# Optimization experiments

Hardware: AMD Instinct MI355X
Metric: run time of the kernel (lower is better)

## Reference

```python
import jax, jax.numpy as jnp
import numpy as np
from math import factorial

N_NODES = 20000
N_EDGES = 80000
NUM_GRAPHS = 64
NUM_NEIGHBORS = 3.8
POOL_NODES = 4.0  # num_nodes=4 constant in source forward

# ---------------- real Wigner 3j (e3nn-style, Frobenius norm 1) ----------------

def _w3j_complex(j1, j2, j3, m1, m2, m3):
    if m1 + m2 + m3 != 0:
        return 0.0
    t1 = j2 - m1 - j3; t2 = j1 + m2 - j3; t3 = j1 + j2 - j3
    t4 = j1 - m1; t5 = j2 + m2
    tmin = max(0, t1, t2); tmax = min(t3, t4, t5)
    if tmin > tmax:
        return 0.0
    s = 0.0
    for t in range(tmin, tmax + 1):
        s += (-1.0) ** t / (factorial(t) * factorial(t - t1) * factorial(t - t2)
                            * factorial(t3 - t) * factorial(t4 - t) * factorial(t5 - t))
    tri = (factorial(j1 + j2 - j3) * factorial(j1 - j2 + j3) * factorial(-j1 + j2 + j3)
           / factorial(j1 + j2 + j3 + 1))
    norm = np.sqrt(tri * factorial(j1 + m1) * factorial(j1 - m1) * factorial(j2 + m2)
                   * factorial(j2 - m2) * factorial(j3 + m3) * factorial(j3 - m3))
    return (-1.0) ** (j1 - j2 - m3) * norm * s


def _real_basis(l):
    U = np.zeros((2 * l + 1, 2 * l + 1), dtype=np.complex128)
    U[l, l] = 1.0
    for m in range(1, l + 1):
        U[l + m, l + m] = (-1) ** m / np.sqrt(2.0)
        U[l + m, l - m] = 1.0 / np.sqrt(2.0)
        U[l - m, l - m] = 1j / np.sqrt(2.0)
        U[l - m, l + m] = -1j * (-1) ** m / np.sqrt(2.0)
    return U

_W3J_CACHE = {}

def w3j(l1, l2, l3):
    key = (l1, l2, l3)
    if key not in _W3J_CACHE:
        C = np.zeros((2 * l1 + 1, 2 * l2 + 1, 2 * l3 + 1), dtype=np.complex128)
        for m1 in range(-l1, l1 + 1):
            for m2 in range(-l2, l2 + 1):
                m3 = -(m1 + m2)
                if -l3 <= m3 <= l3:
                    C[m1 + l1, m2 + l2, m3 + l3] = _w3j_complex(l1, l2, l3, m1, m2, m3)
        C = np.einsum('ia,jb,kc,abc->ijk', _real_basis(l1), _real_basis(l2), _real_basis(l3), C)
        C = np.real((-1j) ** (l1 + l2 + l3) * C)
        _W3J_CACHE[key] = jnp.asarray(C, dtype=jnp.float32)
    return _W3J_CACHE[key]

# ---------------- irreps bookkeeping ----------------
SH        = [(1, 0, 1), (1, 1, -1), (1, 2, 1), (1, 3, -1)]            # 1x0e+1x1o+1x2e+1x3o (dim 16)
GATE1_IN  = [(16,0,1),(16,0,-1),(8,0,1),(8,0,-1),(8,0,1),(8,0,-1),(16,1,-1),(16,1,1)]  # dim 160
GATE1_OUT = [(16,0,1),(16,0,1),(16,1,-1),(16,1,1)]                     # dim 128
GATE2_IN  = [(16,0,1),(16,0,-1),(6,0,1),(6,0,-1),(6,0,1),(6,0,-1),(12,1,-1),(12,1,1)]  # dim 128
GATE2_OUT = [(16,0,1),(16,0,1),(12,1,-1),(12,1,1)]                     # dim 104
OUT_FINAL = [(1, 0, 1)]


def slices(irreps):
    out = []; o = 0
    for m, l, p in irreps:
        d = m * (2 * l + 1); out.append((o, o + d)); o += d
    return out


def tp_paths(ir1, ir2, iro):
    paths = []
    for i1, (m1, l1, p1) in enumerate(ir1):
        for i2, (m2, l2, p2) in enumerate(ir2):
            for io, (mo, lo, po) in enumerate(iro):
                if po == p1 * p2 and abs(l1 - l2) <= lo <= l1 + l2:
                    paths.append((i1, i2, io))
    fan = [0] * len(iro)
    for i1, i2, io in paths:
        fan[io] += ir1[i1][0] * ir2[i2][0]
    numel = sum(ir1[i1][0] * ir2[i2][0] * iro[io][0] for i1, i2, io in paths)
    return paths, fan, numel


def tensor_product(x1, x2, weights, ir1, ir2, iro):
    # FullyConnectedTensorProduct, component norm, element path normalization
    paths, fan, numel = tp_paths(ir1, ir2, iro)
    s1, s2 = slices(ir1), slices(ir2)
    E = x1.shape[0]
    out_parts = [jnp.zeros((E, m * (2 * l + 1)), x1.dtype) for m, l, p in iro]
    wofs = 0
    for i1, i2, io in paths:
        m1, l1, _ = ir1[i1]; m2, l2, _ = ir2[i2]; mo, lo, _ = iro[io]
        n = m1 * m2 * mo
        w = weights[:, wofs:wofs + n].reshape(E, m1, m2, mo); wofs += n
        a = x1[:, s1[i1][0]:s1[i1][1]].reshape(E, m1, 2 * l1 + 1)
        b = x2[:, s2[i2][0]:s2[i2][1]].reshape(E, m2, 2 * l2 + 1)
        C = w3j(l1, l2, lo)
        pw = np.sqrt((2 * lo + 1) / fan[io])
        seg = jnp.einsum('eui,evj,ijk,euvw->ewk', a, b, C, w) * pw
        out_parts[io] = out_parts[io] + seg.reshape(E, mo * (2 * lo + 1))
    return jnp.concatenate(out_parts, axis=1)

# ---------------- activations / gate ----------------
_xs = np.linspace(-8.0, 8.0, 100001)
_pdf = np.exp(-0.5 * _xs ** 2) / np.sqrt(2 * np.pi)
TANH_NORM = float(1.0 / np.sqrt(np.sum(np.tanh(_xs) ** 2 * _pdf) * (_xs[1] - _xs[0])))
SQRT2 = float(np.sqrt(2.0))
ACT = {'relu': lambda t: jnp.maximum(t, 0.0) * SQRT2,
       'abs':  lambda t: jnp.abs(t),
       'tanh': lambda t: jnp.tanh(t) * TANH_NORM}


def gate_fn(x, scalars, gates, gated):
    o = 0; outs = []
    for m, a in scalars:
        outs.append(ACT[a](x[:, o:o + m])); o += m
    gv = []
    for m, a in gates:
        gv.append(ACT[a](x[:, o:o + m])); o += m
    g = jnp.concatenate(gv, axis=-1)
    gi = 0
    for m, l in gated:
        d = 2 * l + 1
        feat = x[:, o:o + m * d].reshape(-1, m, d)
        outs.append((feat * g[:, gi:gi + m, None]).reshape(-1, m * d))
        o += m * d; gi += m
    return jnp.concatenate(outs, axis=-1)

# ---------------- edge features ----------------

def sh_component(v):
    # real spherical harmonics l=0..3, 'component' normalization, unit input
    x, y, z = v[:, 0], v[:, 1], v[:, 2]
    s3, s5, s15 = np.sqrt(3.0), np.sqrt(5.0), np.sqrt(15.0)
    s7, s42, s70, s105 = np.sqrt(7.0), np.sqrt(42.0), np.sqrt(70.0), np.sqrt(105.0)
    Y0 = jnp.ones_like(x)[:, None]
    Y1 = jnp.stack([s3 * y, s3 * z, s3 * x], -1)
    Y2 = jnp.stack([s15 * x * y, s15 * y * z, 0.5 * s5 * (3 * z * z - 1.0),
                    s15 * x * z, 0.5 * s15 * (x * x - y * y)], -1)
    Y3 = jnp.stack([0.25 * s70 * y * (3 * x * x - y * y), s105 * x * y * z,
                    0.25 * s42 * y * (5 * z * z - 1.0), 0.5 * s7 * z * (5 * z * z - 3.0),
                    0.25 * s42 * x * (5 * z * z - 1.0), 0.5 * s105 * z * (x * x - y * y),
                    0.25 * s70 * x * (x * x - 3 * y * y)], -1)
    return jnp.concatenate([Y0, Y1, Y2, Y3], -1)  # [E,16]


def soft_one_hot(r):
    # soft_one_hot_linspace(start=0.5,end=2.5,number=3,basis='smooth_finite',cutoff=True)
    values = np.linspace(0.5, 2.5, 5)[1:-1]
    step = values[1] - values[0]
    diff = (r[:, None] - values) / step
    def f(u):
        return jnp.where(u > 0, jnp.exp(-1.0 / jnp.where(u > 0, u, 1.0)), 0.0)
    y = 1.14136 * np.exp(2.0) * f(diff + 1.0) * f(1.0 - diff)
    return y * np.sqrt(3.0)


def fc(x, w1, w2):
    # e3nn FullyConnectedNet([3,256,numel], relu)
    h = jnp.maximum(x @ (w1 / np.sqrt(w1.shape[0])), 0.0) * SQRT2
    return h @ (w2 / np.sqrt(w2.shape[0]))


def convolution(node_feats, edge_src, edge_dst, edge_attr, edge_scalars, w1, w2, ir_in, ir_out, n_nodes):
    weight = fc(edge_scalars, w1, w2)                                   # [E, numel]
    ef = tensor_product(node_feats[edge_src], edge_attr, weight, ir_in, SH, ir_out)
    return jax.ops.segment_sum(ef, edge_dst, num_segments=n_nodes) / np.sqrt(NUM_NEIGHBORS)


def _forward(pos, w1_1, w2_1, w1_2, w2_2, w1_3, w2_3, edge_src, edge_dst, batch):
    N = pos.shape[0]
    vec = pos[edge_src] - pos[edge_dst]
    r = jnp.sqrt(jnp.sum(vec * vec, axis=1) + 1e-12)
    unit = vec / r[:, None]
    edge_attr = sh_component(unit)
    edge_scalars = soft_one_hot(r)
    x = jax.ops.segment_sum(edge_attr, edge_dst, num_segments=N) / np.sqrt(NUM_NEIGHBORS)
    x = convolution(x, edge_src, edge_dst, edge_attr, edge_scalars, w1_1, w2_1, SH, GATE1_IN, N)
    x = gate_fn(x, [(16, 'relu'), (16, 'abs')], [(8, 'relu'), (8, 'tanh'), (8, 'relu'), (8, 'tanh')], [(16, 1), (16, 1)])
    x = convolution(x, edge_src, edge_dst, edge_attr, edge_scalars, w1_2, w2_2, GATE1_OUT, GATE2_IN, N)
    x = gate_fn(x, [(16, 'relu'), (16, 'abs')], [(6, 'relu'), (6, 'tanh'), (6, 'relu'), (6, 'tanh')], [(12, 1), (12, 1)])
    x = convolution(x, edge_src, edge_dst, edge_attr, edge_scalars, w1_3, w2_3, GATE2_OUT, OUT_FINAL, N)
    x = jax.ops.segment_sum(x, batch, num_segments=NUM_GRAPHS) / np.sqrt(POOL_NODES)
    return jax.nn.sigmoid(x)


def setup_inputs():
    key = jax.random.key(0)
    ks = jax.random.split(key, 10)
    pos = jax.random.normal(ks[0], (N_NODES, 3), jnp.float32) * 1.5
    edge_src = jax.random.randint(ks[1], (N_EDGES,), 0, N_NODES)
    edge_dst = jax.random.randint(ks[2], (N_EDGES,), 0, N_NODES)
    batch = jnp.sort(jax.random.randint(ks[3], (N_NODES,), 0, NUM_GRAPHS))
    _, _, n1 = tp_paths(SH, SH, GATE1_IN)
    _, _, n2 = tp_paths(GATE1_OUT, SH, GATE2_IN)
    _, _, n3 = tp_paths(GATE2_OUT, SH, OUT_FINAL)
    w1_1 = jax.random.normal(ks[4], (3, 256), jnp.float32)
    w2_1 = jax.random.normal(ks[5], (256, n1), jnp.float32)
    w1_2 = jax.random.normal(ks[6], (3, 256), jnp.float32)
    w2_2 = jax.random.normal(ks[7], (256, n2), jnp.float32)
    w1_3 = jax.random.normal(ks[8], (3, 256), jnp.float32)
    w2_3 = jax.random.normal(ks[9], (256, n3), jnp.float32)
    return {'pos': pos, 'w1_1': w1_1, 'w2_1': w2_1, 'w1_2': w1_2, 'w2_2': w2_2,
            'w1_3': w1_3, 'w2_3': w2_3, 'edge_src': edge_src, 'edge_dst': edge_dst, 'batch': batch}


def reference(pos, w1_1, w2_1, w1_2, w2_2, w1_3, w2_3, edge_src, edge_dst, batch):
    return _forward(pos, w1_1, w2_1, w1_2, w2_2, w1_3, w2_3, edge_src, edge_dst, batch)
```

## Files before the change

### kernel.cpp

```cpp
#include <hip/hip_runtime.h>
#include <math.h>

#define NNODE 20000
#define NEDGE 80000
#define NGRAPH 64

#define OFF_TANH  656
#define OFF_CNT   660
#define OFF_GSUM  664
#define OFF_HIST  7680
#define OFF_OFFS  9728
#define OFF_CUR   11784
#define OFF_EATTR 14336
#define OFF_RBUF  1294336
#define OFF_EINFO 1374336
#define OFF_X0    1694336
#define OFF_Y1    2014336
#define OFF_Y2    5214336
#define OFF_X1    7774336
#define OFF_X2    10334336
#define OFF_TAB   12414336

#define T000 0
#define T110 1
#define T220 10
#define T330 35
#define T011 84
#define T101 93
#define T111 102
#define T121 129
#define T211 174
#define T231 219
#define T321 324
#define T221 429
#define T331 504

#define INV_SQRT_NEIGH 0.5129891760425771f
#define SQRT2F 1.4142135623730951f

struct TabD { int l1,l2,l3,off; };
constexpr TabD HTABS[13] = {
  {0,0,0,T000},{1,1,0,T110},{2,2,0,T220},{3,3,0,T330},
  {0,1,1,T011},{1,0,1,T101},{1,1,1,T111},{1,2,1,T121},
  {2,1,1,T211},{2,3,1,T231},{3,2,1,T321},{2,2,1,T221},{3,3,1,T331}
};

struct CoreD { short a_off, b_off; short l1,l2,l3; short tab; short coff; short m1; };
struct PathD { short core; short wofs, wend, ooff; short mo, lo; float pw; };

constexpr CoreD HCORES1[13] = {
  {0,0, 0,0,0, T000, 0, 1},
  {0,1, 0,1,1, T011, 1, 1},
  {1,0, 1,0,1, T101, 4, 1},
  {1,1, 1,1,0, T110, 7, 1},
  {1,1, 1,1,1, T111, 8, 1},
  {1,4, 1,2,1, T121, 11, 1},
  {4,1, 2,1,1, T211, 14, 1},
  {4,4, 2,2,0, T220, 17, 1},
  {4,4, 2,2,1, T221, 18, 1},
  {4,9, 2,3,1, T231, 21, 1},
  {9,4, 3,2,1, T321, 24, 1},
  {9,9, 3,3,0, T330, 27, 1},
  {9,9, 3,3,1, T331, 28, 1}
};
#define PWR 0.7071067811865476f
constexpr PathD HPATHS1[21] = {
  {0,  0, 16,  0,16,0,0.5f},
  {0, 16, 24, 32, 8,0,0.5f},
  {0, 24, 32, 48, 8,0,0.5f},
  {1, 32, 48, 64,16,1,PWR},
  {2, 48, 64, 64,16,1,PWR},
  {3, 64, 80,  0,16,0,0.5f},
  {3, 80, 88, 32, 8,0,0.5f},
  {3, 88, 96, 48, 8,0,0.5f},
  {4, 96,112,112,16,1,1.0f},
  {5,112,128, 64,16,1,PWR},
  {6,128,144, 64,16,1,PWR},
  {7,144,160,  0,16,0,0.5f},
  {7,160,168, 32, 8,0,0.5f},
  {7,168,176, 48, 8,0,0.5f},
  {8,176,192,112,16,1,1.0f},
  {9,192,208, 64,16,1,PWR},
  {10,208,224,64,16,1,PWR},
  {11,224,240, 0,16,0,0.5f},
  {11,240,248,32, 8,0,0.5f},
  {11,248,256,48, 8,0,0.5f},
  {12,256,272,112,16,1,1.0f}
};

constexpr CoreD HCORES2[12] = {
  {0,0,  0,0,0, T000, 0,   16},
  {0,1,  0,1,1, T011, 16,  16},
  {16,0, 0,0,0, T000, 64,  16},
  {16,1, 0,1,1, T011, 80,  16},
  {32,0, 1,0,1, T101, 128, 16},
  {32,1, 1,1,0, T110, 176, 16},
  {32,1, 1,1,1, T111, 192, 16},
  {32,4, 1,2,1, T121, 240, 16},
  {80,0, 1,0,1, T101, 288, 16},
  {80,1, 1,1,0, T110, 336, 16},
  {80,1, 1,1,1, T111, 352, 16},
  {80,4, 1,2,1, T121, 400, 16}
};
#define PA 0.14433756729740643f
#define PB 0.25f
#define PC 0.19364916731037085f
constexpr PathD HPATHS2[20] = {
  {0,   0, 256,  0,16,0,PA},
  {0, 256, 352, 32, 6,0,PA},
  {0, 352, 448, 44, 6,0,PA},
  {1, 448, 640, 56,12,1,PC},
  {2, 640, 896,  0,16,0,PA},
  {2, 896, 992, 32, 6,0,PA},
  {2, 992,1088, 44, 6,0,PA},
  {3,1088,1280, 56,12,1,PC},
  {4,1280,1472, 56,12,1,PC},
  {5,1472,1728,  0,16,0,PA},
  {5,1728,1824, 32, 6,0,PA},
  {5,1824,1920, 44, 6,0,PA},
  {6,1920,2112, 92,12,1,PB},
  {7,2112,2304, 56,12,1,PC},
  {8,2304,2496, 92,12,1,PB},
  {9,2496,2752, 16,16,0,PB},
  {9,2752,2848, 38, 6,0,PB},
  {9,2848,2944, 50, 6,0,PB},
  {10,2944,3136,56,12,1,PC},
  {11,3136,3328,92,12,1,PB}
};

constexpr CoreD HCORES3[3] = {
  {0,0,  0,0,0, T000, 0,  16},
  {16,0, 0,0,0, T000, 16, 16},
  {32,1, 1,1,0, T110, 32, 12}
};
#define PD 0.15075567228888181f
constexpr PathD HPATHS3[3] = {
  {0, 0,16, 0,1,0,PD},
  {1,16,32, 0,1,0,PD},
  {2,32,44, 0,1,0,PD}
};

constexpr double FACT[9] = {1.0,1.0,2.0,6.0,24.0,120.0,720.0,5040.0,40320.0};

constexpr double csqrt_(double x){
  if(x<=0.0) return 0.0;
  double g = (x<1.0)? 1.0 : x;
  for(int i=0;i<40;i++) g = 0.5*(g + x/g);
  return g;
}

constexpr double cw3j_(int j1,int j2,int j3,int m1,int m2,int m3){
  if(m1+m2+m3!=0) return 0.0;
  int t1=j2-m1-j3, t2=j1+m2-j3, t3=j1+j2-j3, t4=j1-m1, t5=j2+m2;
  int tmin=t1>0?t1:0; if(t2>tmin) tmin=t2;
  int tmax=t3<t4?t3:t4; if(t5<tmax) tmax=t5;
  if(tmin>tmax) return 0.0;
  double s=0.0;
  for(int t=tmin;t<=tmax;++t){
    double d=FACT[t]*FACT[t-t1]*FACT[t-t2]*FACT[t3-t]*FACT[t4-t]*FACT[t5-t];
    s += ((t&1)? -1.0:1.0)/d;
  }
  double tri=FACT[j1+j2-j3]*FACT[j1-j2+j3]*FACT[-j1+j2+j3]/FACT[j1+j2+j3+1];
  double nrm=csqrt_(tri*FACT[j1+m1]*FACT[j1-m1]*FACT[j2+m2]*FACT[j2-m2]*FACT[j3+m3]*FACT[j3-m3]);
  return (((j1-j2-m3)&1)? -1.0:1.0)*nrm*s;
}

constexpr int curow_(int l,int i,int* a,double* re,double* im){
  const double is2=0.7071067811865475;
  int m=i-l;
  if(m==0){ a[0]=l; re[0]=1.0; im[0]=0.0; return 1; }
  if(m>0){
    a[0]=l+m; re[0]=((m&1)? -is2:is2); im[0]=0.0;
    a[1]=l-m; re[1]=is2; im[1]=0.0; return 2;
  }
  int mm=-m;
  a[0]=l-mm; re[0]=0.0; im[0]=is2;
  a[1]=l+mm; re[1]=0.0; im[1]=((mm&1)? is2:-is2);
  return 2;
}

constexpr float cw3j_elem_(int l1,int l2,int l3,int i,int j,int k){
  int aa[2]={0,0},bb[2]={0,0},cc[2]={0,0};
  double ar[2]={0,0},ai[2]={0,0},br[2]={0,0},bi[2]={0,0},cr[2]={0,0},ci[2]={0,0};
  int na=curow_(l1,i,aa,ar,ai);
  int nb=curow_(l2,j,bb,br,bi);
  int nc=curow_(l3,k,cc,cr,ci);
  double accr=0.0, acci=0.0;
  for(int x=0;x<na;x++)for(int y=0;y<nb;y++)for(int w=0;w<nc;w++){
    double wv=cw3j_(l1,l2,l3, aa[x]-l1, bb[y]-l2, cc[w]-l3);
    if(wv==0.0) continue;
    double pr=ar[x]*br[y]-ai[x]*bi[y];
    double pi=ar[x]*bi[y]+ai[x]*br[y];
    double qr=pr*cr[w]-pi*ci[w];
    double qi=pr*ci[w]+pi*cr[w];
    accr+=qr*wv; acci+=qi*wv;
  }
  int Lm=(l1+l2+l3)&3;
  double res = (Lm==0)? accr : (Lm==1)? acci : (Lm==2)? -accr : -acci;
  return (float)res;
}

struct WApart { float v[429]; };
constexpr WApart gen_wa_(){
  WApart o{};
  for(int t=0;t<11;t++){
    int l1=HTABS[t].l1,l2=HTABS[t].l2,l3=HTABS[t].l3;
    int n2=2*l2+1,n3=2*l3+1;
    int tot=(2*l1+1)*n2*n3;
    for(int z=0;z<tot;z++){
      int i=z/(n2*n3), j=(z/n3)%n2, k=z%n3;
      o.v[HTABS[t].off+z]=cw3j_elem_(l1,l2,l3,i,j,k);
    }
  }
  return o;
}
struct WBpart { float v[222]; };
constexpr WBpart gen_wb_(){
  WBpart o{};
  for(int t=11;t<13;t++){
    int l1=HTABS[t].l1,l2=HTABS[t].l2,l3=HTABS[t].l3;
    int n2=2*l2+1,n3=2*l3+1;
    int tot=(2*l1+1)*n2*n3;
    for(int z=0;z<tot;z++){
      int i=z/(n2*n3), j=(z/n3)%n2, k=z%n3;
      o.v[HTABS[t].off-429+z]=cw3j_elem_(l1,l2,l3,i,j,k);
    }
  }
  return o;
}
constexpr WApart WAC = gen_wa_();
constexpr WBpart WBC = gen_wb_();
struct W3Full { float v[651]; };
constexpr W3Full gen_wfull_(){
  W3Full f{};
  for(int i=0;i<429;i++) f.v[i]=WAC.v[i];
  for(int i=0;i<222;i++) f.v[429+i]=WBC.v[i];
  return f;
}
__constant__ W3Full W3JC = gen_wfull_();

template<int NW> struct PwArr { float v[NW]; };
template<int NW,int NP>
constexpr PwArr<NW> gen_pw_(const PathD (&P)[NP]){
  PwArr<NW> a{};
  for(int p=0;p<NP;p++)
    for(int j=P[p].wofs;j<P[p].wend;j++) a.v[j]=P[p].pw;
  return a;
}
__constant__ PwArr<272>  PWC1 = gen_pw_<272>(HPATHS1);
__constant__ PwArr<3328> PWC2 = gen_pw_<3328>(HPATHS2);
__constant__ PwArr<44>   PWC3 = gen_pw_<44>(HPATHS3);

struct OutSeg { int mult, l; };
constexpr OutSeg OSEG1[8] = {{16,0},{16,0},{8,0},{8,0},{8,0},{8,0},{16,1},{16,1}};
constexpr OutSeg OSEG2[8] = {{16,0},{16,0},{6,0},{6,0},{6,0},{6,0},{12,1},{12,1}};
constexpr OutSeg OSEG3[1] = {{1,0}};

struct Ent2 { int jb, cb, nu; };
template<int NCOL,int NENT,int NW> struct ColMetaT {
  int cidx[NCOL+1];
  int obase[NCOL];
  int n3c[NCOL];
  Ent2 ent[NENT];
  int newj[NW];
};

template<int NCOL,int NENT,int NW,int NSEG,int NP,int NC>
constexpr ColMetaT<NCOL,NENT,NW> gen_colmeta_(const OutSeg (&S)[NSEG], const PathD (&P)[NP], const CoreD (&C)[NC]){
  ColMetaT<NCOL,NENT,NW> m{};
  int col=0, cnt=0, o=0, nb=0;
  for(int s=0;s<NSEG;s++){
    int n3=2*S[s].l+1;
    for(int wc=0;wc<S[s].mult;wc++){
      m.cidx[col]=cnt;
      int ob=o+wc*n3;
      m.obase[col]=ob;
      m.n3c[col]=n3;
      for(int p=0;p<NP;p++){
        PathD pd=P[p];
        int pn3=2*pd.lo+1;
        if(pn3!=n3) continue;
        int rel=ob-pd.ooff;
        if(rel<0||rel>=pd.mo*pn3) continue;
        int w=rel/pn3;
        CoreD cd=C[pd.core];
        int m1=cd.m1;
        m.ent[cnt]=Ent2{nb,(int)cd.coff,m1};
        for(int u=0;u<m1;u++) m.newj[pd.wofs + w + u*pd.mo]=nb+u;
        nb+=m1;
        cnt++;
      }
      col++;
    }
    o+=S[s].mult*n3;
  }
  m.cidx[col]=cnt;
  return m;
}

__constant__ ColMetaT<96,272,272>  CMETA1 = gen_colmeta_<96,272,272>(OSEG1, HPATHS1, HCORES1);
__constant__ ColMetaT<80,208,3328> CMETA2 = gen_colmeta_<80,208,3328>(OSEG2, HPATHS2, HCORES2);
__constant__ ColMetaT< 1,  3,  44> CMETA3 = gen_colmeta_< 1,  3,  44>(OSEG3, HPATHS3, HCORES3);

struct CItem { short aoff, boff, n1, n2, cofs, jstep, woff, pad; };
struct CArr1 { CItem it[31]; };
constexpr CArr1 gen_c1_(){
  CArr1 a{}; int s=0;
  for(int cn=0;cn<13;cn++){
    CoreD cd=HCORES1[cn];
    int n1=2*cd.l1+1,n2=2*cd.l2+1,n3=2*cd.l3+1;
    for(int k=0;k<n3;k++){
      a.it[s]=CItem{cd.a_off,cd.b_off,(short)n1,(short)n2,(short)(cd.tab+k),(short)n3,(short)(cd.coff+k),0};
      s++;
    }
  }
  return a;
}
__constant__ CArr1 CIT1 = gen_c1_();

struct Fam { short b_off, tab, n1, n2, n3, goff; };
constexpr Fam GF2[6]={
  {0,T000,1,1,1,0},{1,T011,1,3,3,1},{0,T101,3,1,3,4},
  {1,T110,3,3,1,13},{1,T111,3,3,3,16},{4,T121,3,5,3,25}};
constexpr Fam GF3[2]={{0,T000,1,1,1,0},{1,T110,3,3,1,1}};
struct CoreG { short fam,a_off,m1,coff; };
constexpr CoreG CG2[12]={
  {0,0,16,0},{1,0,16,16},{0,16,16,64},{1,16,16,80},
  {2,32,16,128},{3,32,16,176},{4,32,16,192},{5,32,16,240},
  {2,80,16,288},{3,80,16,336},{4,80,16,352},{5,80,16,400}};
constexpr CoreG CG3[3]={{0,0,16,0},{0,16,16,16},{1,32,12,32}};

struct GItem { short boff, cofs, n2, jstep; };
template<int NG> struct GArrT { GItem it[NG]; };
template<int NG,int NF>
constexpr GArrT<NG> gen_g_(const Fam (&F)[NF]){
  GArrT<NG> a{}; int s=0;
  for(int f=0;f<NF;f++){
    for(int i=0;i<F[f].n1;i++)for(int k=0;k<F[f].n3;k++){
      a.it[s]=GItem{F[f].b_off,(short)(F[f].tab + i*F[f].n2*F[f].n3 + k),F[f].n2,F[f].n3};
      s++;
    }
  }
  return a;
}
__constant__ GArrT<34> GIT2=gen_g_<34>(GF2);
__constant__ GArrT<4>  GIT3=gen_g_<4>(GF3);

struct OItem { short aoff, gofs, n1, n3, woff, pad; };
template<int NO> struct OArrT { OItem it[NO]; };
template<int NO,int NC,int NF>
constexpr OArrT<NO> gen_o_(const CoreG (&C)[NC], const Fam (&F)[NF]){
  OArrT<NO> a{}; int s=0;
  for(int cn=0;cn<NC;cn++){
    Fam f=F[C[cn].fam];
    for(int k=0;k<f.n3;k++)for(int u=0;u<C[cn].m1;u++){
      a.it[s]=OItem{(short)(C[cn].a_off+u*f.n1),(short)(f.goff+k),f.n1,f.n3,
                    (short)(C[cn].coff+k*C[cn].m1+u),0};
      s++;
    }
  }
  return a;
}
__constant__ OArrT<448> OIT2=gen_o_<448,12,6>(CG2,GF2);
__constant__ OArrT<44>  OIT3=gen_o_<44,3,2>(CG3,GF3);

template<int CNT,int N3,int NCOLS>
__device__ __forceinline__ void apply1_col(const Ent2* __restrict__ ep, const float* __restrict__ T0,
    const float* __restrict__ crb, float fr, float&a0,float&a1,float&a2){
  const float* tja=T0+ep[0].jb;
  float wv[CNT];
  #pragma unroll
  for(int t=0;t<CNT;t++){
    float w0=tja[t], w1=tja[t+NCOLS];
    wv[t]=w0+fr*(w1-w0);
  }
  #pragma unroll
  for(int t=0;t<CNT;t++){
    const float* cr=crb+ep[t].cb;
    a0=fmaf(wv[t],cr[0],a0);
    if constexpr(N3==3){ a1=fmaf(wv[t],cr[1],a1); a2=fmaf(wv[t],cr[2],a2); }
  }
}
__device__ __forceinline__ void apply1_dyn(const Ent2* __restrict__ ep, int cnt, int n3,
    const float* __restrict__ T0, const float* __restrict__ crb, float fr, int NCOLS,
    float&a0,float&a1,float&a2){
  const float* tja=T0+ep[0].jb;
  for(int t=0;t<cnt;t++){
    float w0=tja[t], w1=tja[t+NCOLS];
    float w=w0+fr*(w1-w0);
    const float* cr=crb+ep[t].cb;
    a0=fmaf(w,cr[0],a0);
    if(n3==3){ a1=fmaf(w,cr[1],a1); a2=fmaf(w,cr[2],a2); }
  }
}
template<int CNT,int N3,int NCOLS>
__device__ __forceinline__ void apply2_col(const Ent2* __restrict__ ep, const float* __restrict__ T0,
    const float* __restrict__ crb, float fr, float&a0,float&a1,float&a2){
  #pragma unroll
  for(int t=0;t<CNT;t++){
    const float* cr=crb+ep[t].cb;
    const float* tj=T0+ep[t].jb;
    #pragma unroll
    for(int uu=0;uu<16;uu+=4){
      float4 w0=*(const float4*)(tj+uu);
      float4 w1=*(const float4*)(tj+NCOLS+uu);
      float w;
      if constexpr(N3==1){
        float4 cv=*(const float4*)(cr+uu);
        w=w0.x+fr*(w1.x-w0.x); a0=fmaf(w,cv.x,a0);
        w=w0.y+fr*(w1.y-w0.y); a0=fmaf(w,cv.y,a0);
        w=w0.z+fr*(w1.z-w0.z); a0=fmaf(w,cv.z,a0);
        w=w0.w+fr*(w1.w-w0.w); a0=fmaf(w,cv.w,a0);
      } else {
        float4 c0=*(const float4*)(cr+uu);
        float4 c1=*(const float4*)(cr+16+uu);
        float4 c2=*(const float4*)(cr+32+uu);
        w=w0.x+fr*(w1.x-w0.x); a0=fmaf(w,c0.x,a0); a1=fmaf(w,c1.x,a1); a2=fmaf(w,c2.x,a2);
        w=w0.y+fr*(w1.y-w0.y); a0=fmaf(w,c0.y,a0); a1=fmaf(w,c1.y,a1); a2=fmaf(w,c2.y,a2);
        w=w0.z+fr*(w1.z-w0.z); a0=fmaf(w,c0.z,a0); a1=fmaf(w,c1.z,a1); a2=fmaf(w,c2.z,a2);
        w=w0.w+fr*(w1.w-w0.w); a0=fmaf(w,c0.w,a0); a1=fmaf(w,c1.w,a1); a2=fmaf(w,c2.w,a2);
      }
    }
  }
}
__device__ __forceinline__ void apply2_dyn(const Ent2* __restrict__ ep, int cnt, int n3,
    const float* __restrict__ T0, const float* __restrict__ crb, float fr, int NCOLS,
    float&a0,float&a1,float&a2){
  for(int t=0;t<cnt;t++){
    const float* cr=crb+ep[t].cb;
    const float* tj=T0+ep[t].jb;
    #pragma unroll
    for(int uu=0;uu<16;uu+=4){
      float4 w0=*(const float4*)(tj+uu);
      float4 w1=*(const float4*)(tj+NCOLS+uu);
      float w;
      if(n3==1){
        float4 cv=*(const float4*)(cr+uu);
        w=w0.x+fr*(w1.x-w0.x); a0=fmaf(w,cv.x,a0);
        w=w0.y+fr*(w1.y-w0.y); a0=fmaf(w,cv.y,a0);
        w=w0.z+fr*(w1.z-w0.z); a0=fmaf(w,cv.z,a0);
        w=w0.w+fr*(w1.w-w0.w); a0=fmaf(w,cv.w,a0);
      } else {
        float4 c0=*(const float4*)(cr+uu);
        float4 c1=*(const float4*)(cr+16+uu);
        float4 c2=*(const float4*)(cr+32+uu);
        w=w0.x+fr*(w1.x-w0.x); a0=fmaf(w,c0.x,a0); a1=fmaf(w,c1.x,a1); a2=fmaf(w,c2.x,a2);
        w=w0.y+fr*(w1.y-w0.y); a0=fmaf(w,c0.y,a0); a1=fmaf(w,c1.y,a1); a2=fmaf(w,c2.y,a2);
        w=w0.z+fr*(w1.z-w0.z); a0=fmaf(w,c0.z,a0); a1=fmaf(w,c1.z,a1); a2=fmaf(w,c2.z,a2);
        w=w0.w+fr*(w1.w-w0.w); a0=fmaf(w,c0.w,a0); a1=fmaf(w,c1.w,a1); a2=fmaf(w,c2.w,a2);
      }
    }
  }
}

template<int JT>
__device__ __forceinline__ void table_gemm(const float* __restrict__ W2, float* __restrict__ tab,
    int NCOLS, float scale, const float* __restrict__ PW, const int* __restrict__ NJ,
    int jb, const float (*__restrict__ sh_h)[8], int r0, int R){
  float acc[8][JT];
  #pragma unroll
  for(int k=0;k<8;k++)
    #pragma unroll
    for(int u=0;u<JT;u++) acc[k][u]=0.0f;
  const float* w2p=W2+jb;
  float w0[JT], w1[JT];
  *(float4*)&w0[0]=*(const float4*)(w2p);
  *(float4*)&w1[0]=*(const float4*)(w2p+NCOLS);
  if constexpr(JT==8){
    *(float4*)&w0[4]=*(const float4*)(w2p+4);
    *(float4*)&w1[4]=*(const float4*)(w2p+NCOLS+4);
  }
  for(int c=0;c<256;c+=2){
    int cp0=(c+2<256)?(c+2):255;
    int cp1=(c+3<256)?(c+3):255;
    float n0[JT], n1[JT];
    *(float4*)&n0[0]=*(const float4*)(w2p+(size_t)cp0*NCOLS);
    *(float4*)&n1[0]=*(const float4*)(w2p+(size_t)cp1*NCOLS);
    if constexpr(JT==8){
      *(float4*)&n0[4]=*(const float4*)(w2p+(size_t)cp0*NCOLS+4);
      *(float4*)&n1[4]=*(const float4*)(w2p+(size_t)cp1*NCOLS+4);
    }
    float h0[8], h1[8];
    *(float4*)&h0[0]=*(const float4*)&sh_h[c][0];
    *(float4*)&h0[4]=*(const float4*)&sh_h[c][4];
    *(float4*)&h1[0]=*(const float4*)&sh_h[c+1][0];
    *(float4*)&h1[4]=*(const float4*)&sh_h[c+1][4];
    #pragma unroll
    for(int k=0;k<8;k++)
      #pragma unroll
      for(int u=0;u<JT;u++)
        acc[k][u]=fmaf(h0[k],w0[u],acc[k][u]);
    #pragma unroll
    for(int k=0;k<8;k++)
      #pragma unroll
      for(int u=0;u<JT;u++)
        acc[k][u]=fmaf(h1[k],w1[u],acc[k][u]);
    #pragma unroll
    for(int u=0;u<JT;u++){ w0[u]=n0[u]; w1[u]=n1[u]; }
  }
  #pragma unroll
  for(int u=0;u<JT;u++){
    float cs=scale*PW[jb+u];
    int jn=NJ[jb+u];
    #pragma unroll
    for(int k=0;k<8;k++){
      int ri=r0+k;
      if(ri<R) tab[(size_t)ri*NCOLS+jn]=acc[k][u]*cs;
    }
  }
}

__global__ __launch_bounds__(512) void k_tables(
    const float* __restrict__ W1_1, const float* __restrict__ W2_1, float* __restrict__ T1,
    const float* __restrict__ W1_2, const float* __restrict__ W2_2, float* __restrict__ T2,
    const float* __restrict__ W1_3, const float* __restrict__ W2_3, float* __restrict__ T3,
    int R, int NR, float* __restrict__ ws){
  int tid=threadIdx.x;
  int by=blockIdx.y;
  if(by==4){
    if(blockIdx.x!=0) return;
    for(int i=tid;i<(728-OFF_CNT);i+=512) ws[OFF_CNT+i]=0.0f;
    for(int i=tid;i<(13832-OFF_HIST);i+=512) ws[OFF_HIST+i]=0.0f;
    __shared__ double red[512];
    double loc=0.0;
    for(int i=tid;i<=100000;i+=512){
      float x=-8.0f+16.0f*(float)i/100000.0f;
      float th=tanhf(x);
      float pdf=expf(-0.5f*x*x)*0.3989422804014327f;
      loc += (double)(th*th*pdf);
    }
    red[tid]=loc; __syncthreads();
    for(int s=256;s>0;s>>=1){ if(tid<s) red[tid]+=red[tid+s]; __syncthreads(); }
    if(tid==0) ws[OFF_TANH]=(float)(1.0/sqrt(red[0]*(16.0/100000.0)));
    return;
  }
  int conv, jb0;
  const float* W1; const float* W2; float* tab; int NCOLS; float scale;
  if(by==0){ conv=2; jb0=0;    W1=W1_2; W2=W2_2; tab=T2; NCOLS=3328; scale=INV_SQRT_NEIGH; }
  else if(by==1){ conv=2; jb0=2048; W1=W1_2; W2=W2_2; tab=T2; NCOLS=3328; scale=INV_SQRT_NEIGH; }
  else if(by==2){ conv=1; jb0=0; W1=W1_1; W2=W2_1; tab=T1; NCOLS=272;  scale=INV_SQRT_NEIGH; }
  else { conv=3; jb0=0; W1=W1_3; W2=W2_3; tab=T3; NCOLS=44;   scale=INV_SQRT_NEIGH*0.5f; }

  __shared__ float sh_h[256][8];
  int r0=blockIdx.x*8;
  if(tid<256){
    int c=tid;
    float wa=W1[c], wb=W1[256+c], wc=W1[512+c];
    const float A=(float)(1.14136*7.38905609893065*1.7320508075688772);
    #pragma unroll
    for(int k=0;k<8;k++){
      int ri=r0+k;
      float r=0.5f+2.0f*(float)ri/(float)NR;
      float sv[3];
      #pragma unroll
      for(int j=0;j<3;j++){
        float v=1.0f+0.5f*(float)j;
        float diff=(r-v)*2.0f;
        float u1=diff+1.0f, u2=1.0f-diff;
        float f1=(u1>0.0f)? expf(-1.0f/u1):0.0f;
        float f2=(u2>0.0f)? expf(-1.0f/u2):0.0f;
        sv[j]=A*f1*f2;
      }
      float hv=sv[0]*wa+sv[1]*wb+sv[2]*wc;
      hv=fmaxf(hv*0.5773502691896258f,0.0f)*(SQRT2F*0.0625f);
      sh_h[c][k]=hv;
    }
  }
  __syncthreads();
  const float* PW=(conv==1)? PWC1.v : (conv==2)? PWC2.v : PWC3.v;
  const int* NJ=(conv==1)? CMETA1.newj : (conv==2)? CMETA2.newj : CMETA3.newj;
  int jb=jb0+tid*4;
  if(jb+4<=((conv==2)? ((jb0==0)?2048:NCOLS) : NCOLS))
    table_gemm<4>(W2,tab,NCOLS,scale,PW,NJ,jb,sh_h,r0,R);
}

__global__ void k_edge(const float* __restrict__ pos, const int* __restrict__ esrc,
                       const int* __restrict__ edst, float* __restrict__ ws, int NR){
  int e = blockIdx.x*256 + threadIdx.x;
  if(e>=NEDGE) return;
  float* eattr=ws+OFF_EATTR;
  float* x0=ws+OFF_X0;
  int s=esrc[e], d=edst[e];
  float x=pos[3*s]-pos[3*d], y=pos[3*s+1]-pos[3*d+1], z=pos[3*s+2]-pos[3*d+2];
  float r=sqrtf(x*x+y*y+z*z+1e-12f);
  float iv=1.0f/r; x*=iv; y*=iv; z*=iv;
  const float s3=1.7320508075688772f, s5=2.2360679774997896f, s15=3.872983346207417f;
  const float s7=2.6457513110645907f, s42=6.48074069840786f, s70=8.366600265340756f, s105=10.246950765959598f;
  float Y[16];
  Y[0]=1.0f;
  Y[1]=s3*y; Y[2]=s3*z; Y[3]=s3*x;
  Y[4]=s15*x*y; Y[5]=s15*y*z; Y[6]=0.5f*s5*(3.0f*z*z-1.0f); Y[7]=s15*x*z; Y[8]=0.5f*s15*(x*x-y*y);
  Y[9]=0.25f*s70*y*(3.0f*x*x-y*y); Y[10]=s105*x*y*z; Y[11]=0.25f*s42*y*(5.0f*z*z-1.0f);
  Y[12]=0.5f*s7*z*(5.0f*z*z-3.0f); Y[13]=0.25f*s42*x*(5.0f*z*z-1.0f);
  Y[14]=0.5f*s105*z*(x*x-y*y); Y[15]=0.25f*s70*x*(x*x-3.0f*y*y);
  float4* ep=(float4*)(eattr+(size_t)e*16);
  ep[0]=make_float4(Y[0],Y[1],Y[2],Y[3]);
  ep[1]=make_float4(Y[4],Y[5],Y[6],Y[7]);
  ep[2]=make_float4(Y[8],Y[9],Y[10],Y[11]);
  ep[3]=make_float4(Y[12],Y[13],Y[14],Y[15]);
  #pragma unroll
  for(int i=0;i<16;i++)
    atomicAdd(&x0[(size_t)d*16+i], Y[i]*INV_SQRT_NEIGH);
  ws[OFF_RBUF+e]=r;
  if(r>0.5f && r<2.5f){
    float t=(r-0.5f)*((float)NR*0.5f);
    int i0=min((int)t, NR-1);
    atomicAdd((int*)(ws+OFF_HIST)+i0, 1);
  }
}

__global__ void k_scan(float* __restrict__ ws, int NR){
  __shared__ int sd[2048];
  int t=threadIdx.x;
  int* hist=(int*)(ws+OFF_HIST);
  int* offs=(int*)(ws+OFF_OFFS);
  int i1=t, i2=t+1024;
  sd[i1]=(i1<NR)? hist[i1]:0;
  sd[i2]=(i2<NR)? hist[i2]:0;
  __syncthreads();
  for(int d=1; d<2048; d<<=1){
    int v1=(i1>=d)? sd[i1-d]:0;
    int v2=(i2>=d)? sd[i2-d]:0;
    __syncthreads();
    sd[i1]+=v1; sd[i2]+=v2;
    __syncthreads();
  }
  if(i1<NR) offs[i1]=(i1==0)?0:sd[i1-1];
  if(i2<NR) offs[i2]=sd[i2-1];
  if(t==0){ offs[NR]=sd[NR-1]; *((int*)(ws+OFF_CNT))=sd[NR-1]; }
}

__global__ void k_scatter(const int* __restrict__ esrc, const int* __restrict__ edst,
                          float* __restrict__ ws, int NR){
  int e=blockIdx.x*256+threadIdx.x;
  if(e>=NEDGE) return;
  float r=ws[OFF_RBUF+e];
  if(!(r>0.5f && r<2.5f)) return;
  float t=(r-0.5f)*((float)NR*0.5f);
  int i0=min((int)t, NR-1);
  int* offs=(int*)(ws+OFF_OFFS);
  int* cur=(int*)(ws+OFF_CUR);
  int p=offs[i0]+atomicAdd(&cur[i0],1);
  int4 v; v.x=esrc[e]; v.y=edst[e]; v.z=e; v.w=__float_as_int(t);
  ((int4*)(ws+OFF_EINFO))[p]=v;
}

template<int CONV,int DY,int D_IN,int D_OUT,int CSTRIDE,int NCOL,int NCOLS,bool FINAL>
__global__ __launch_bounds__(256,4) void k_conv(
    const float* __restrict__ xin, const float* __restrict__ TAB,
    float* __restrict__ yout, const int* __restrict__ batchp,
    float* __restrict__ ws, int NR)
{
  constexpr int APAD = D_IN+4;
  constexpr int NGP  = (CONV==2)?36:4;
  constexpr int YST  = (CONV==3)?132:4;
  constexpr int NGV  = (CONV==2)?32:((CONV==3)?24:1);
  __shared__ float sh_a[8][APAD];
  __shared__ float sh_b[8][20];
  __shared__ float sh_core[8][CSTRIDE];
  __shared__ float sh_g[8][NGP];
  __shared__ float sh_gv[8][NGV];
  __shared__ float sh_y[8][YST];
  __shared__ float sh_red[8];
  __shared__ int sh_src[8], sh_dst[8], sh_eid[8];
  __shared__ float sh_t[8];

  int tid=threadIdx.x;
  int nact=*(const int*)(ws+OFF_CNT);
  int base=blockIdx.x*8;
  if(base>=nact) return;
  int ne=min(8, nact-base);

  if(tid<8){
    int src=0,dst=0,eid=-1; float tv=0.0f;
    if(tid<ne){
      int4 v=((const int4*)(ws+OFF_EINFO))[base+tid];
      src=v.x; dst=v.y; eid=v.z; tv=__int_as_float(v.w);
    }
    sh_src[tid]=src; sh_dst[tid]=dst; sh_eid[tid]=eid; sh_t[tid]=tv;
    if constexpr(CONV==3) sh_red[tid]=0.0f;
  }
  __syncthreads();

  if(tid<32){
    int idx=tid>>2, c4=tid&3;
    int eid=sh_eid[idx];
    float4 v=make_float4(0.f,0.f,0.f,0.f);
    if(eid>=0) v=((const float4*)(ws+OFF_EATTR+(size_t)eid*16))[c4];
    *(float4*)&sh_b[idx][c4*4]=v;
  }
  if constexpr(CONV==1){
    if(tid>=32 && tid<64){
      int t2=tid-32; int idx=t2>>2, c4=t2&3;
      float4 v=make_float4(0.f,0.f,0.f,0.f);
      if(sh_eid[idx]>=0) v=((const float4*)(xin+(size_t)sh_src[idx]*16))[c4];
      *(float4*)&sh_a[idx][c4*4]=v;
    }
  } else {
    constexpr int YQ=DY/4;
    for(int z=tid; z<8*YQ; z+=256){
      int idx=z/YQ, c4=z-idx*YQ;
      float4 v=make_float4(0.f,0.f,0.f,0.f);
      if(sh_eid[idx]>=0) v=((const float4*)(xin+(size_t)sh_src[idx]*DY))[c4];
      if constexpr(CONV==2) *(float4*)&sh_core[idx][c4*4]=v;
      else                  *(float4*)&sh_y[idx][c4*4]=v;
    }
  }
  __syncthreads();

  if constexpr(CONV==1){
    constexpr int NIT=31;
    for(int z=tid; z<8*NIT; z+=256){
      int idx=z/NIT, rem=z-idx*NIT;
      CItem it=CIT1.it[rem];
      float acc=0.0f;
      for(int i=0;i<it.n1;i++){
        float av=sh_a[idx][it.aoff+i];
        int cb=it.cofs + i*it.n2*it.jstep;
        for(int j=0;j<it.n2;j++)
          acc += av*sh_b[idx][it.boff+j]*W3JC.v[cb + j*it.jstep];
      }
      sh_core[idx][it.woff]=acc;
    }
    __syncthreads();
  } else {
    float TN=ws[OFF_TANH];
    for(int z=tid; z<8*NGV; z+=256){
      int idx=z/NGV, m=z-idx*NGV;
      const float* yr=(CONV==2)? &sh_core[idx][0] : &sh_y[idx][0];
      float u=yr[32+m];
      bool th=(CONV==2)? (((m>>3)&1)!=0) : (((m/6)&1)!=0);
      sh_gv[idx][m]= th? tanhf(u)*TN : fmaxf(u,0.0f)*SQRT2F;
    }
    constexpr int NG=(CONV==2)?34:4;
    for(int z=tid; z<8*NG; z+=256){
      int idx=z/NG, rem=z-idx*NG;
      GItem it=(CONV==2)? GIT2.it[rem] : GIT3.it[rem];
      float acc=0.0f;
      for(int j=0;j<it.n2;j++)
        acc += sh_b[idx][it.boff+j]*W3JC.v[it.cofs + j*it.jstep];
      sh_g[idx][rem]=acc;
    }
    __syncthreads();
    for(int z=tid; z<8*D_IN; z+=256){
      int idx=z/D_IN, o=z-idx*D_IN;
      const float* yr=(CONV==2)? &sh_core[idx][0] : &sh_y[idx][0];
      float val;
      if(o<16) val=fmaxf(yr[o],0.0f)*SQRT2F;
      else if(o<32) val=fabsf(yr[o]);
      else {
        if constexpr(CONV==2){
          int gi=(o<80)? (o-32)/3 : 16+(o-80)/3;
          val=yr[o+32]*sh_gv[idx][gi];
        } else {
          int gi=(o<68)? (o-32)/3 : 12+(o-68)/3;
          val=yr[o+24]*sh_gv[idx][gi];
        }
      }
      sh_a[idx][o]=val;
    }
    __syncthreads();
    constexpr int NO=(CONV==2)?448:44;
    for(int z=tid; z<8*NO; z+=256){
      int idx=z/NO, rem=z-idx*NO;
      OItem it=(CONV==2)? OIT2.it[rem] : OIT3.it[rem];
      float acc=0.0f;
      #pragma unroll 3
      for(int i=0;i<it.n1;i++)
        acc += sh_a[idx][it.aoff+i]*sh_g[idx][it.gofs + i*it.n3];
      sh_core[idx][it.woff]=acc;
    }
    __syncthreads();
  }

  if constexpr(CONV==3){
    if(tid<88){
      int e3=tid&7, c=tid>>3;
      float tv=sh_t[e3];
      int i0=min((int)tv, NR-1);
      float fr=tv-(float)i0;
      const float* tj=TAB+(size_t)i0*NCOLS + c*4;
      float4 w0=*(const float4*)tj;
      float4 w1=*(const float4*)(tj+NCOLS);
      float4 cv=*(const float4*)(&sh_core[e3][c*4]);
      float p;
      p  = (w0.x+fr*(w1.x-w0.x))*cv.x;
      p += (w0.y+fr*(w1.y-w0.y))*cv.y;
      p += (w0.z+fr*(w1.z-w0.z))*cv.z;
      p += (w0.w+fr*(w1.w-w0.w))*cv.w;
      atomicAdd(&sh_red[e3], p);
    }
    __syncthreads();
    if(tid<ne) atomicAdd(&ws[OFF_GSUM+batchp[sh_dst[tid]]], sh_red[tid]);
  } else {
    int e=tid&7;
    float tv=sh_t[e];
    int i0=min((int)tv, NR-1);
    float fr=tv-(float)i0;
    const float* T0=TAB+(size_t)i0*NCOLS;
    const float* crb=&sh_core[e][0];
    int dstv=sh_dst[e];
    bool act=(e<ne);

    for(int q=tid; q<8*NCOL; q+=256){
      int c=q>>3;
      int s0,s1,ob,n3;
      const Ent2* entp;
      if constexpr(CONV==1){ s0=CMETA1.cidx[c]; s1=CMETA1.cidx[c+1]; ob=CMETA1.obase[c]; n3=CMETA1.n3c[c]; entp=CMETA1.ent; }
      else                 { s0=CMETA2.cidx[c]; s1=CMETA2.cidx[c+1]; ob=CMETA2.obase[c]; n3=CMETA2.n3c[c]; entp=CMETA2.ent; }
      int cnt=s1-s0;
      if(!cnt) continue;
      float a0=0.0f,a1=0.0f,a2=0.0f;
      const Ent2* ep=entp+s0;
      if constexpr(CONV==1){
        if(n3==1){
          switch(cnt){
            case 4: apply1_col<4,1,272>(ep,T0,crb,fr,a0,a1,a2); break;
            default: apply1_dyn(ep,cnt,1,T0,crb,fr,272,a0,a1,a2); break;
          }
        } else {
          switch(cnt){
            case 6: apply1_col<6,3,272>(ep,T0,crb,fr,a0,a1,a2); break;
            case 3: apply1_col<3,3,272>(ep,T0,crb,fr,a0,a1,a2); break;
            default: apply1_dyn(ep,cnt,3,T0,crb,fr,272,a0,a1,a2); break;
          }
        }
      } else {
        if(n3==1){
          switch(cnt){
            case 3: apply2_col<3,1,3328>(ep,T0,crb,fr,a0,a1,a2); break;
            case 1: apply2_col<1,1,3328>(ep,T0,crb,fr,a0,a1,a2); break;
            default: apply2_dyn(ep,cnt,1,T0,crb,fr,3328,a0,a1,a2); break;
          }
        } else {
          switch(cnt){
            case 5: apply2_col<5,3,3328>(ep,T0,crb,fr,a0,a1,a2); break;
            case 3: apply2_col<3,3,3328>(ep,T0,crb,fr,a0,a1,a2); break;
            default: apply2_dyn(ep,cnt,3,T0,crb,fr,3328,a0,a1,a2); break;
          }
        }
      }
      if(act){
        float* yp=&yout[(size_t)dstv*D_OUT+ob];
        atomicAdd(yp, a0);
        if(n3==3){ atomicAdd(yp+1, a1); atomicAdd(yp+2, a2); }
      }
    }
  }
}

__global__ void k_sig(const float* __restrict__ ws, float* __restrict__ out){
  int g=threadIdx.x;
  if(g<NGRAPH){
    float v=ws[OFF_GSUM+g];
    out[g]=1.0f/(1.0f+expf(-v));
  }
}

extern "C" void kernel_launch(void* const* d_in, const int* in_sizes, int n_in,
                              void* d_out, int out_size, void* d_ws, size_t ws_size,
                              hipStream_t stream){
  const float* pos =(const float*)d_in[0];
  const float* w1_1=(const float*)d_in[1];
  const float* w2_1=(const float*)d_in[2];
  const float* w1_2=(const float*)d_in[3];
  const float* w2_2=(const float*)d_in[4];
  const float* w1_3=(const float*)d_in[5];
  const float* w2_3=(const float*)d_in[6];
  const int* esrc=(const int*)d_in[7];
  const int* edst=(const int*)d_in[8];
  const int* batch=(const int*)d_in[9];
  float* ws=(float*)d_ws;
  float* out=(float*)d_out;

  long availRows = ((long)(ws_size/4) - (long)OFF_TAB)/3644L;
  int R = (availRows < 1025L)? (int)availRows : 1025;
  if(R < 9) R = 9;
  int NR = R-1;
  float* TAB1 = ws + OFF_TAB;
  float* TAB2 = TAB1 + (size_t)R*272;
  float* TAB3 = TAB2 + (size_t)R*3328;

  hipMemsetAsync(ws+OFF_X0, 0, (size_t)(OFF_X1-OFF_X0)*sizeof(float), stream);

  k_tables<<<dim3((R+7)/8,5),512,0,stream>>>(
      w1_1,w2_1,TAB1, w1_2,w2_2,TAB2, w1_3,w2_3,TAB3, R,NR, ws);
  k_edge<<<(NEDGE+255)/256,256,0,stream>>>(pos, esrc, edst, ws, NR);
  k_scan<<<1,1024,0,stream>>>(ws, NR);
  k_scatter<<<(NEDGE+255)/256,256,0,stream>>>(esrc, edst, ws, NR);

  k_conv<1, 16, 16,160, 33, 96, 272,false><<<(NEDGE+7)/8,256,0,stream>>>(
      ws+OFF_X0, TAB1, ws+OFF_Y1, batch, ws, NR);

  k_conv<2,160,128,128,452, 80,3328,false><<<(NEDGE+7)/8,256,0,stream>>>(
      ws+OFF_Y1, TAB2, ws+OFF_Y2, batch, ws, NR);

  k_conv<3,128,104,  1, 68,  1, 44,true ><<<(NEDGE+7)/8,256,0,stream>>>(
      ws+OFF_Y2, TAB3, nullptr, batch, ws, NR);

  k_sig<<<1,64,0,stream>>>(ws, out);
}
```

Measured before the change: 376.0 us.

## Split table GEMM across more blocks and break FMA dependency chain in scalar apply

```diff
diff --git a/kernel.cpp b/kernel.cpp
--- a/kernel.cpp
+++ b/kernel.cpp
@@ -396,25 +396,38 @@
 template<int CNT,int N3,int NCOLS>
 __device__ __forceinline__ void apply2_col(const Ent2* __restrict__ ep, const float* __restrict__ T0,
     const float* __restrict__ crb, float fr, float&a0,float&a1,float&a2){
-  #pragma unroll
-  for(int t=0;t<CNT;t++){
-    const float* cr=crb+ep[t].cb;
-    const float* tj=T0+ep[t].jb;
+  if constexpr(N3==1){
+    float s0=0.0f,s1=0.0f,s2=0.0f,s3=0.0f;
     #pragma unroll
-    for(int uu=0;uu<16;uu+=4){
-      float4 w0=*(const float4*)(tj+uu);
-      float4 w1=*(const float4*)(tj+NCOLS+uu);
-      float w;
-      if constexpr(N3==1){
+    for(int t=0;t<CNT;t++){
+      const float* cr=crb+ep[t].cb;
+      const float* tj=T0+ep[t].jb;
+      #pragma unroll
+      for(int uu=0;uu<16;uu+=4){
+        float4 w0=*(const float4*)(tj+uu);
+        float4 w1=*(const float4*)(tj+NCOLS+uu);
         float4 cv=*(const float4*)(cr+uu);
-        w=w0.x+fr*(w1.x-w0.x); a0=fmaf(w,cv.x,a0);
-        w=w0.y+fr*(w1.y-w0.y); a0=fmaf(w,cv.y,a0);
-        w=w0.z+fr*(w1.z-w0.z); a0=fmaf(w,cv.z,a0);
-        w=w0.w+fr*(w1.w-w0.w); a0=fmaf(w,cv.w,a0);
-      } else {
+        float w;
+        w=w0.x+fr*(w1.x-w0.x); s0=fmaf(w,cv.x,s0);
+        w=w0.y+fr*(w1.y-w0.y); s1=fmaf(w,cv.y,s1);
+        w=w0.z+fr*(w1.z-w0.z); s2=fmaf(w,cv.z,s2);
+        w=w0.w+fr*(w1.w-w0.w); s3=fmaf(w,cv.w,s3);
+      }
+    }
+    a0=(s0+s1)+(s2+s3);
+  } else {
+    #pragma unroll
+    for(int t=0;t<CNT;t++){
+      const float* cr=crb+ep[t].cb;
+      const float* tj=T0+ep[t].jb;
+      #pragma unroll
+      for(int uu=0;uu<16;uu+=4){
+        float4 w0=*(const float4*)(tj+uu);
+        float4 w1=*(const float4*)(tj+NCOLS+uu);
         float4 c0=*(const float4*)(cr+uu);
         float4 c1=*(const float4*)(cr+16+uu);
         float4 c2=*(const float4*)(cr+32+uu);
+        float w;
         w=w0.x+fr*(w1.x-w0.x); a0=fmaf(w,c0.x,a0); a1=fmaf(w,c1.x,a1); a2=fmaf(w,c2.x,a2);
         w=w0.y+fr*(w1.y-w0.y); a0=fmaf(w,c0.y,a0); a1=fmaf(w,c1.y,a1); a2=fmaf(w,c2.y,a2);
         w=w0.z+fr*(w1.z-w0.z); a0=fmaf(w,c0.z,a0); a1=fmaf(w,c1.z,a1); a2=fmaf(w,c2.z,a2);
@@ -454,6 +467,12 @@
 }
 
 template<int JT>
+__device__ __forceinline__ void ldw_(float* w, const float* p){
+  if constexpr(JT==2) *(float2*)w = *(const float2*)p;
+  else if constexpr(JT==4) *(float4*)w = *(const float4*)p;
+  else { *(float4*)w=*(const float4*)p; *(float4*)(w+4)=*(const float4*)(p+4); }
+}
+template<int JT>
 __device__ __forceinline__ void table_gemm(const float* __restrict__ W2, float* __restrict__ tab,
     int NCOLS, float scale, const float* __restrict__ PW, const int* __restrict__ NJ,
     int jb, const float (*__restrict__ sh_h)[8], int r0, int R){
@@ -464,22 +483,14 @@
     for(int u=0;u<JT;u++) acc[k][u]=0.0f;
   const float* w2p=W2+jb;
   float w0[JT], w1[JT];
-  *(float4*)&w0[0]=*(const float4*)(w2p);
-  *(float4*)&w1[0]=*(const float4*)(w2p+NCOLS);
-  if constexpr(JT==8){
-    *(float4*)&w0[4]=*(const float4*)(w2p+4);
-    *(float4*)&w1[4]=*(const float4*)(w2p+NCOLS+4);
-  }
+  ldw_<JT>(w0, w2p);
+  ldw_<JT>(w1, w2p+NCOLS);
   for(int c=0;c<256;c+=2){
     int cp0=(c+2<256)?(c+2):255;
     int cp1=(c+3<256)?(c+3):255;
     float n0[JT], n1[JT];
-    *(float4*)&n0[0]=*(const float4*)(w2p+(size_t)cp0*NCOLS);
-    *(float4*)&n1[0]=*(const float4*)(w2p+(size_t)cp1*NCOLS);
-    if constexpr(JT==8){
-      *(float4*)&n0[4]=*(const float4*)(w2p+(size_t)cp0*NCOLS+4);
-      *(float4*)&n1[4]=*(const float4*)(w2p+(size_t)cp1*NCOLS+4);
-    }
+    ldw_<JT>(n0, w2p+(size_t)cp0*NCOLS);
+    ldw_<JT>(n1, w2p+(size_t)cp1*NCOLS);
     float h0[8], h1[8];
     *(float4*)&h0[0]=*(const float4*)&sh_h[c][0];
     *(float4*)&h0[4]=*(const float4*)&sh_h[c][4];
@@ -510,40 +521,40 @@
   }
 }
 
-__global__ __launch_bounds__(512) void k_tables(
+__global__ __launch_bounds__(256) void k_tables(
     const float* __restrict__ W1_1, const float* __restrict__ W2_1, float* __restrict__ T1,
     const float* __restrict__ W1_2, const float* __restrict__ W2_2, float* __restrict__ T2,
     const float* __restrict__ W1_3, const float* __restrict__ W2_3, float* __restrict__ T3,
     int R, int NR, float* __restrict__ ws){
   int tid=threadIdx.x;
   int by=blockIdx.y;
-  if(by==4){
+  if(by==9){
     if(blockIdx.x!=0) return;
-    for(int i=tid;i<(728-OFF_CNT);i+=512) ws[OFF_CNT+i]=0.0f;
-    for(int i=tid;i<(13832-OFF_HIST);i+=512) ws[OFF_HIST+i]=0.0f;
-    __shared__ double red[512];
+    for(int i=tid;i<(728-OFF_CNT);i+=256) ws[OFF_CNT+i]=0.0f;
+    for(int i=tid;i<(13832-OFF_HIST);i+=256) ws[OFF_HIST+i]=0.0f;
+    __shared__ double red[256];
     double loc=0.0;
-    for(int i=tid;i<=100000;i+=512){
+    for(int i=tid;i<=100000;i+=256){
       float x=-8.0f+16.0f*(float)i/100000.0f;
       float th=tanhf(x);
       float pdf=expf(-0.5f*x*x)*0.3989422804014327f;
       loc += (double)(th*th*pdf);
     }
     red[tid]=loc; __syncthreads();
-    for(int s=256;s>0;s>>=1){ if(tid<s) red[tid]+=red[tid+s]; __syncthreads(); }
+    for(int s=128;s>0;s>>=1){ if(tid<s) red[tid]+=red[tid+s]; __syncthreads(); }
     if(tid==0) ws[OFF_TANH]=(float)(1.0/sqrt(red[0]*(16.0/100000.0)));
     return;
   }
-  int conv, jb0;
+  int conv, jb0, jlim;
   const float* W1; const float* W2; float* tab; int NCOLS; float scale;
-  if(by==0){ conv=2; jb0=0;    W1=W1_2; W2=W2_2; tab=T2; NCOLS=3328; scale=INV_SQRT_NEIGH; }
-  else if(by==1){ conv=2; jb0=2048; W1=W1_2; W2=W2_2; tab=T2; NCOLS=3328; scale=INV_SQRT_NEIGH; }
-  else if(by==2){ conv=1; jb0=0; W1=W1_1; W2=W2_1; tab=T1; NCOLS=272;  scale=INV_SQRT_NEIGH; }
-  else { conv=3; jb0=0; W1=W1_3; W2=W2_3; tab=T3; NCOLS=44;   scale=INV_SQRT_NEIGH*0.5f; }
+  if(by<7){ conv=2; jb0=by*512; jlim=(jb0+512<3328)?(jb0+512):3328;
+            W1=W1_2; W2=W2_2; tab=T2; NCOLS=3328; scale=INV_SQRT_NEIGH; }
+  else if(by==7){ conv=1; jb0=0; jlim=272; W1=W1_1; W2=W2_1; tab=T1; NCOLS=272;  scale=INV_SQRT_NEIGH; }
+  else { conv=3; jb0=0; jlim=44; W1=W1_3; W2=W2_3; tab=T3; NCOLS=44;   scale=INV_SQRT_NEIGH*0.5f; }
 
   __shared__ float sh_h[256][8];
   int r0=blockIdx.x*8;
-  if(tid<256){
+  {
     int c=tid;
     float wa=W1[c], wb=W1[256+c], wc=W1[512+c];
     const float A=(float)(1.14136*7.38905609893065*1.7320508075688772);
@@ -569,9 +580,9 @@
   __syncthreads();
   const float* PW=(conv==1)? PWC1.v : (conv==2)? PWC2.v : PWC3.v;
   const int* NJ=(conv==1)? CMETA1.newj : (conv==2)? CMETA2.newj : CMETA3.newj;
-  int jb=jb0+tid*4;
-  if(jb+4<=((conv==2)? ((jb0==0)?2048:NCOLS) : NCOLS))
-    table_gemm<4>(W2,tab,NCOLS,scale,PW,NJ,jb,sh_h,r0,R);
+  int jb=jb0+tid*2;
+  if(jb+2<=jlim)
+    table_gemm<2>(W2,tab,NCOLS,scale,PW,NJ,jb,sh_h,r0,R);
 }
 
 __global__ void k_edge(const float* __restrict__ pos, const int* __restrict__ esrc,
@@ -883,7 +894,7 @@
 
   hipMemsetAsync(ws+OFF_X0, 0, (size_t)(OFF_X1-OFF_X0)*sizeof(float), stream);
 
-  k_tables<<<dim3((R+7)/8,5),512,0,stream>>>(
+  k_tables<<<dim3((R+7)/8,10),256,0,stream>>>(
       w1_1,w2_1,TAB1, w1_2,w2_2,TAB2, w1_3,w2_3,TAB3, R,NR, ws);
   k_edge<<<(NEDGE+255)/256,256,0,stream>>>(pos, esrc, edst, ws, NR);
   k_scan<<<1,1024,0,stream>>>(ws, NR);
```

Measured after the change: 396.3 us. +5.4%, slower.
